# Kernel tuning notes

Hardware: AMD Instinct MI355X
Metric: run time of the kernel (lower is better)

Reference implementation:

```python
import jax, jax.numpy as jnp
import numpy as np

N, C, E, H = 10000, 128, 640000, 8


def setup_inputs() -> dict:
    key = jax.random.key(0)
    k1, k2, k3, k4, k5 = jax.random.split(key, 5)
    x = jax.random.normal(k1, (N, C), dtype=jnp.float32)
    edge_index = jax.random.randint(k2, (2, E), 0, N, dtype=jnp.int64)
    edge_attr = jax.random.uniform(k3, (E,), dtype=jnp.float32)
    W = jax.random.normal(k4, (2 * C, H), dtype=jnp.float32) * (1.0 / np.sqrt(2 * C))
    b = jax.random.normal(k5, (H,), dtype=jnp.float32) * 0.01
    return {"x": x, "edge_index": edge_index, "edge_attr": edge_attr, "W": W, "b": b}


def reference(x, edge_index, edge_attr, W, b):
    row, col = edge_index[0], edge_index[1]
    # Split W so we never materialize the concatenated [E, 2C] tensor:
    # cat([x[row], x[col]]) @ W == x[row] @ W[:C] + x[col] @ W[C:]
    Wr, Wc = W[:x.shape[1]], W[x.shape[1]:]
    logits = x[row] @ Wr + x[col] @ Wc + b          # [E, H]
    alpha = jax.nn.sigmoid(logits) * edge_attr[:, None]
    self_loop = (row == col)[:, None]                # [E, 1] -> broadcast over heads
    alpha = jnp.where(self_loop, jnp.ones((), dtype=alpha.dtype), alpha)
    return (alpha, edge_index)
```

## Files before the change

kernel.cpp:

```cpp
#include <hip/hip_runtime.h>

#define N_NODES   10000
#define C_DIM     128
#define H_DIM     8
#define YZ_TOTAL  (N_NODES * H_DIM)
#define YZ_BLOCKS ((N_NODES * 32) / 256)

typedef _Float16 h2 __attribute__((ext_vector_type(2)));
typedef _Float16 h8 __attribute__((ext_vector_type(8)));
typedef float    fx4 __attribute__((ext_vector_type(4)));

__global__ void __launch_bounds__(256)
k1_yz_and_index(const float* __restrict__ x, const float* __restrict__ W,
                const float* __restrict__ b, const int* __restrict__ ei,
                float* __restrict__ out, _Float16* __restrict__ yzh, int E) {
    const int bid = blockIdx.x;

    if (bid < YZ_BLOCKS) {
        const int t = bid * 256 + threadIdx.x;
        const int n = t >> 5;
        if (n >= N_NODES) return;
        const int w  = t & 31;
        const int s  = w >> 2;
        const int hp = w & 3;
        const int h0 = hp * 2;

        const float4* xr4 = (const float4*)(x + (size_t)n * C_DIM) + s * 4;
        float4 xv0 = xr4[0], xv1 = xr4[1], xv2 = xr4[2], xv3 = xr4[3];
        const float xk[16] = { xv0.x,xv0.y,xv0.z,xv0.w, xv1.x,xv1.y,xv1.z,xv1.w,
                               xv2.x,xv2.y,xv2.z,xv2.w, xv3.x,xv3.y,xv3.z,xv3.w };

        const int k0 = s * 16;
        const float* wr = W + (size_t)k0 * H_DIM + h0;
        const float* wc = W + (size_t)(C_DIM + k0) * H_DIM + h0;

        float ar0 = 0.f, ar1 = 0.f, ac0 = 0.f, ac1 = 0.f;
#pragma unroll
        for (int j = 0; j < 16; ++j) {
            float2 wr2 = *(const float2*)(wr + j * H_DIM);
            float2 wc2 = *(const float2*)(wc + j * H_DIM);
            ar0 = fmaf(xk[j], wr2.x, ar0);
            ar1 = fmaf(xk[j], wr2.y, ar1);
            ac0 = fmaf(xk[j], wc2.x, ac0);
            ac1 = fmaf(xk[j], wc2.y, ac1);
        }
#pragma unroll
        for (int m = 4; m <= 16; m <<= 1) {
            ar0 += __shfl_xor(ar0, m, 64);
            ar1 += __shfl_xor(ar1, m, 64);
            ac0 += __shfl_xor(ac0, m, 64);
            ac1 += __shfl_xor(ac1, m, 64);
        }
        if (s == 0) {
            float2 bb = *(const float2*)(b + h0);
            h2 yv = { (_Float16)(ar0 + bb.x), (_Float16)(ar1 + bb.y) };
            h2 zv = { (_Float16)ac0,          (_Float16)ac1 };
            *(h2*)(yzh + (size_t)n * H_DIM + h0)            = yv;
            *(h2*)(yzh + YZ_TOTAL + (size_t)n * H_DIM + h0) = zv;
        }
    } else {
        const size_t ib = (size_t)E * H_DIM;
        const int t = (bid - YZ_BLOCKS) * 256 + threadIdx.x;
        const int i = t * 4;
        const int total = 2 * E;
        if (i + 3 < total) {
            int4 v = *(const int4*)(ei + i);
            fx4 f = { (float)v.x, (float)v.y, (float)v.z, (float)v.w };
            __builtin_nontemporal_store(f, (fx4*)(out + ib + i));
        } else {
            for (int j = i; j < total; ++j) out[ib + j] = (float)ei[j];
        }
    }
}

__device__ __forceinline__ float sigmoid_fast(float v) {
    return __builtin_amdgcn_rcpf(1.f + __expf(-v));
}

__global__ void edge_alpha(const int* __restrict__ ei,
                           const float* __restrict__ ea,
                           const _Float16* __restrict__ yzh,
                           float* __restrict__ out, int E) {
    const int e = blockIdx.x * blockDim.x + threadIdx.x;
    if (e >= E) return;
    int   r = __builtin_nontemporal_load(ei + e);
    int   c = __builtin_nontemporal_load(ei + E + e);
    float a = __builtin_nontemporal_load(ea + e);

    h8 yv = *(const h8*)(yzh + (size_t)r * H_DIM);
    h8 zv = *(const h8*)(yzh + YZ_TOTAL + (size_t)c * H_DIM);

    const bool self = (r == c);
    float res[8];
#pragma unroll
    for (int h = 0; h < 8; ++h) {
        float v = (float)yv[h] + (float)zv[h];
        res[h] = self ? 1.f : sigmoid_fast(v) * a;
    }

    fx4 lo = { res[0], res[1], res[2], res[3] };
    fx4 hi = { res[4], res[5], res[6], res[7] };
    __builtin_nontemporal_store(lo, (fx4*)(out + (size_t)e * H_DIM));
    __builtin_nontemporal_store(hi, (fx4*)(out + (size_t)e * H_DIM + 4));
}

extern "C" void kernel_launch(void* const* d_in, const int* in_sizes, int n_in,
                              void* d_out, int out_size, void* d_ws, size_t ws_size,
                              hipStream_t stream) {
    const float* x  = (const float*)d_in[0];
    const int*   ei = (const int*)d_in[1];
    const float* ea = (const float*)d_in[2];
    const float* W  = (const float*)d_in[3];
    const float* b  = (const float*)d_in[4];
    float* out = (float*)d_out;
    _Float16* yzh = (_Float16*)d_ws;
    const int E = in_sizes[2];

    {
        const int conv_threads = (2 * E + 3) / 4;
        const int conv_blocks  = (conv_threads + 255) / 256;
        const int grid = YZ_BLOCKS + conv_blocks;
        hipLaunchKernelGGL(k1_yz_and_index, dim3(grid), dim3(256), 0, stream,
                           x, W, b, ei, out, yzh, E);
    }
    {
        const int grid = (E + 255) / 256;
        hipLaunchKernelGGL(edge_alpha, dim3(grid), dim3(256), 0, stream,
                           ei, ea, yzh, out, E);
    }
}
```

Baseline: 22.36 us.

## Move edge_index float conversion into edge_alpha kernel to avoid rereading indices

The int-to-float conversion of edge_index leaves the first kernel and is done inside edge_alpha, which already loads row and col for each edge. This drops a second full read of edge_index (about 5 MB) and shrinks the first kernel to just the per-node projection. The x loads in the projection kernel also become nontemporal. In exchange, edge_alpha issues two scalar 4-byte stores per thread instead of the previous vectorised 16-byte stores for the index part of the output.

```diff
diff --git a/kernel.cpp b/kernel.cpp
--- a/kernel.cpp
+++ b/kernel.cpp
@@ -11,65 +11,51 @@
 typedef float    fx4 __attribute__((ext_vector_type(4)));
 
 __global__ void __launch_bounds__(256)
-k1_yz_and_index(const float* __restrict__ x, const float* __restrict__ W,
-                const float* __restrict__ b, const int* __restrict__ ei,
-                float* __restrict__ out, _Float16* __restrict__ yzh, int E) {
-    const int bid = blockIdx.x;
+precompute_yz(const float* __restrict__ x, const float* __restrict__ W,
+              const float* __restrict__ b, _Float16* __restrict__ yzh) {
+    const int t = blockIdx.x * blockDim.x + threadIdx.x;
+    const int n = t >> 5;
+    if (n >= N_NODES) return;
+    const int w  = t & 31;
+    const int s  = w >> 2;
+    const int hp = w & 3;
+    const int h0 = hp * 2;
 
-    if (bid < YZ_BLOCKS) {
-        const int t = bid * 256 + threadIdx.x;
-        const int n = t >> 5;
-        if (n >= N_NODES) return;
-        const int w  = t & 31;
-        const int s  = w >> 2;
-        const int hp = w & 3;
-        const int h0 = hp * 2;
+    const fx4* xr4 = (const fx4*)(x + (size_t)n * C_DIM) + s * 4;
+    fx4 xv0 = __builtin_nontemporal_load(xr4 + 0);
+    fx4 xv1 = __builtin_nontemporal_load(xr4 + 1);
+    fx4 xv2 = __builtin_nontemporal_load(xr4 + 2);
+    fx4 xv3 = __builtin_nontemporal_load(xr4 + 3);
+    const float xk[16] = { xv0.x,xv0.y,xv0.z,xv0.w, xv1.x,xv1.y,xv1.z,xv1.w,
+                           xv2.x,xv2.y,xv2.z,xv2.w, xv3.x,xv3.y,xv3.z,xv3.w };
 
-        const float4* xr4 = (const float4*)(x + (size_t)n * C_DIM) + s * 4;
-        float4 xv0 = xr4[0], xv1 = xr4[1], xv2 = xr4[2], xv3 = xr4[3];
-        const float xk[16] = { xv0.x,xv0.y,xv0.z,xv0.w, xv1.x,xv1.y,xv1.z,xv1.w,
-                               xv2.x,xv2.y,xv2.z,xv2.w, xv3.x,xv3.y,xv3.z,xv3.w };
+    const int k0 = s * 16;
+    const float* wr = W + (size_t)k0 * H_DIM + h0;
+    const float* wc = W + (size_t)(C_DIM + k0) * H_DIM + h0;
 
-        const int k0 = s * 16;
-        const float* wr = W + (size_t)k0 * H_DIM + h0;
-        const float* wc = W + (size_t)(C_DIM + k0) * H_DIM + h0;
-
-        float ar0 = 0.f, ar1 = 0.f, ac0 = 0.f, ac1 = 0.f;
+    float ar0 = 0.f, ar1 = 0.f, ac0 = 0.f, ac1 = 0.f;
 #pragma unroll
-        for (int j = 0; j < 16; ++j) {
-            float2 wr2 = *(const float2*)(wr + j * H_DIM);
-            float2 wc2 = *(const float2*)(wc + j * H_DIM);
-            ar0 = fmaf(xk[j], wr2.x, ar0);
-            ar1 = fmaf(xk[j], wr2.y, ar1);
-            ac0 = fmaf(xk[j], wc2.x, ac0);
-            ac1 = fmaf(xk[j], wc2.y, ac1);
-        }
+    for (int j = 0; j < 16; ++j) {
+        float2 wr2 = *(const float2*)(wr + j * H_DIM);
+        float2 wc2 = *(const float2*)(wc + j * H_DIM);
+        ar0 = fmaf(xk[j], wr2.x, ar0);
+        ar1 = fmaf(xk[j], wr2.y, ar1);
+        ac0 = fmaf(xk[j], wc2.x, ac0);
+        ac1 = fmaf(xk[j], wc2.y, ac1);
+    }
 #pragma unroll
-        for (int m = 4; m <= 16; m <<= 1) {
-            ar0 += __shfl_xor(ar0, m, 64);
-            ar1 += __shfl_xor(ar1, m, 64);
-            ac0 += __shfl_xor(ac0, m, 64);
-            ac1 += __shfl_xor(ac1, m, 64);
-        }
-        if (s == 0) {
-            float2 bb = *(const float2*)(b + h0);
-            h2 yv = { (_Float16)(ar0 + bb.x), (_Float16)(ar1 + bb.y) };
-            h2 zv = { (_Float16)ac0,          (_Float16)ac1 };
-            *(h2*)(yzh + (size_t)n * H_DIM + h0)            = yv;
-            *(h2*)(yzh + YZ_TOTAL + (size_t)n * H_DIM + h0) = zv;
-        }
-    } else {
-        const size_t ib = (size_t)E * H_DIM;
-        const int t = (bid - YZ_BLOCKS) * 256 + threadIdx.x;
-        const int i = t * 4;
-        const int total = 2 * E;
-        if (i + 3 < total) {
-            int4 v = *(const int4*)(ei + i);
-            fx4 f = { (float)v.x, (float)v.y, (float)v.z, (float)v.w };
-            __builtin_nontemporal_store(f, (fx4*)(out + ib + i));
-        } else {
-            for (int j = i; j < total; ++j) out[ib + j] = (float)ei[j];
-        }
+    for (int m = 4; m <= 16; m <<= 1) {
+        ar0 += __shfl_xor(ar0, m, 64);
+        ar1 += __shfl_xor(ar1, m, 64);
+        ac0 += __shfl_xor(ac0, m, 64);
+        ac1 += __shfl_xor(ac1, m, 64);
+    }
+    if (s == 0) {
+        float2 bb = *(const float2*)(b + h0);
+        h2 yv = { (_Float16)(ar0 + bb.x), (_Float16)(ar1 + bb.y) };
+        h2 zv = { (_Float16)ac0,          (_Float16)ac1 };
+        *(h2*)(yzh + (size_t)n * H_DIM + h0)            = yv;
+        *(h2*)(yzh + YZ_TOTAL + (size_t)n * H_DIM + h0) = zv;
     }
 }
 
@@ -77,18 +63,22 @@
     return __builtin_amdgcn_rcpf(1.f + __expf(-v));
 }
 
-__global__ void edge_alpha(const int* __restrict__ ei,
-                           const float* __restrict__ ea,
-                           const _Float16* __restrict__ yzh,
-                           float* __restrict__ out, int E) {
+__global__ void __launch_bounds__(256)
+edge_alpha(const int* __restrict__ ei, const float* __restrict__ ea,
+           const _Float16* __restrict__ yzh, float* __restrict__ out, int E) {
     const int e = blockIdx.x * blockDim.x + threadIdx.x;
     if (e >= E) return;
+    const size_t ib = (size_t)E * H_DIM;
+
     int   r = __builtin_nontemporal_load(ei + e);
     int   c = __builtin_nontemporal_load(ei + E + e);
     float a = __builtin_nontemporal_load(ea + e);
 
     h8 yv = *(const h8*)(yzh + (size_t)r * H_DIM);
     h8 zv = *(const h8*)(yzh + YZ_TOTAL + (size_t)c * H_DIM);
+
+    __builtin_nontemporal_store((float)r, out + ib + e);
+    __builtin_nontemporal_store((float)c, out + ib + E + e);
 
     const bool self = (r == c);
     float res[8];
@@ -117,11 +107,8 @@
     const int E = in_sizes[2];
 
     {
-        const int conv_threads = (2 * E + 3) / 4;
-        const int conv_blocks  = (conv_threads + 255) / 256;
-        const int grid = YZ_BLOCKS + conv_blocks;
-        hipLaunchKernelGGL(k1_yz_and_index, dim3(grid), dim3(256), 0, stream,
-                           x, W, b, ei, out, yzh, E);
+        hipLaunchKernelGGL(precompute_yz, dim3(YZ_BLOCKS), dim3(256), 0, stream,
+                           x, W, b, yzh);
     }
     {
         const int grid = (E + 255) / 256;
```

Result: no change. 22.67 us (+1.4%).
